# Kernel tuning notes

Measured on AMD Instinct MI355X. Metric: run time of the kernel, lower is better.

The kernel has to match this reference:

```python
import jax, jax.numpy as jnp
import numpy as np

B = 32          # graphs per batch
NPG = 512       # nodes per graph
EPG = 2048      # original edges per graph (stored in y[:, -1])
N = B * NPG     # 16384 nodes
E = B * EPG     # 65536 edges
GF = 5          # num_global_features
ETOT = E + N    # edges after add_self_loops

def _lin(k, o, i):
    return jax.random.normal(k, (o, i), jnp.float32) / np.sqrt(i)

def setup_inputs():
    key = jax.random.key(0)
    ks = jax.random.split(key, 20)
    x = jax.random.normal(ks[0], (N,), jnp.float32)
    off = (jnp.arange(B, dtype=jnp.int32) * NPG)[:, None]
    src = (jax.random.randint(ks[1], (B, EPG), 0, NPG, dtype=jnp.int32) + off).reshape(-1)
    dst = (jax.random.randint(ks[2], (B, EPG), 0, NPG, dtype=jnp.int32) + off).reshape(-1)
    edge_index = jnp.stack([src, dst])
    edge_attr = jax.random.normal(ks[3], (E, GF), jnp.float32)
    # last global feature = number of edges per graph (module reads y[:, -1])
    y = jax.random.normal(ks[4], (B, GF), jnp.float32).at[:, -1].set(float(EPG)).reshape(-1)
    batch_vector = jnp.repeat(jnp.arange(B, dtype=jnp.int32), NPG)
    p = dict(
        Wn=_lin(ks[5], 512, 1), bn=jnp.zeros(512, jnp.float32),
        We=_lin(ks[6], 511, GF), be=jnp.zeros(511, jnp.float32),
        Wg=_lin(ks[7], 512, GF), bg=jnp.zeros(512, jnp.float32),
        Wl=_lin(ks[8], 1024, 512), bl=jnp.zeros(1024, jnp.float32),
        Wr=_lin(ks[9], 1024, 512), br=jnp.zeros(1024, jnp.float32),
        Wge=_lin(ks[10], 1024, 511),
        att=jax.random.normal(ks[11], (1024,), jnp.float32) / 32.0,
        bgat=jnp.zeros(1024, jnp.float32),
        Wm=_lin(ks[12], 1024, 1024), bm=jnp.zeros(1024, jnp.float32),
        Wmi=_lin(ks[13], 1024, 1024), bmi=jnp.zeros(1024, jnp.float32),
        Wce=_lin(ks[14], 1024, 512), bce=jnp.zeros(1024, jnp.float32),
        W1=_lin(ks[15], 256, 2048), b1=jnp.zeros(256, jnp.float32),
        W2=_lin(ks[16], 1, 256), b2=jnp.zeros(1, jnp.float32),
    )
    return dict(x=x, edge_index=edge_index, edge_attr=edge_attr, y=y,
                batch_vector=batch_vector, **p)

def _leaky(v, s=0.01):
    return jnp.where(v >= 0, v, s * v)

def _forward(edge_index, batch_vector, x, edge_attr, y, Wn, bn, We, be, Wg, bg,
             Wl, bl, Wr, br, Wge, att, bgat, Wm, bm, Wmi, bmi, Wce, bce,
             W1, b1, W2, b2):
    # add_self_loops (fill_value=1.0 for edge_attr), self loops appended last
    loops = jnp.arange(N, dtype=edge_index.dtype)
    src = jnp.concatenate([edge_index[0], loops])
    dst = jnp.concatenate([edge_index[1], loops])
    ea = jnp.concatenate([edge_attr, jnp.ones((N, GF), edge_attr.dtype)], axis=0)
    # preprocessing MLPs (dropout = identity at inference)
    h = _leaky(x[:, None] @ Wn.T + bn)               # [N, 512]
    e = _leaky(ea @ We.T + be)                       # [ETOT, 511]
    yg = _leaky(y.reshape(B, GF) @ Wg.T + bg)        # [B, 512]
    # GATv2Conv, 1 head, concat, negative_slope=0.2, no self-loop add
    xl = h @ Wl.T + bl                               # source transform [N, 1024]
    xr = h @ Wr.T + br                               # target transform [N, 1024]
    m = _leaky(xl[src] + xr[dst] + e @ Wge.T, 0.2)   # [ETOT, 1024]
    logit = m @ att                                  # [ETOT]
    mx = jax.ops.segment_max(logit, dst, num_segments=N)
    ex = jnp.exp(logit - mx[dst])
    alpha = ex / (jax.ops.segment_sum(ex, dst, num_segments=N)[dst] + 1e-16)
    gat = jax.ops.segment_sum(alpha[:, None] * xl[src], dst, num_segments=N) + bgat
    edge_total = jnp.concatenate([e, alpha[:, None]], axis=1)  # [ETOT, 512]
    # GeneralConv: undirected message, add aggregation, identity skip (in==out)
    hm = gat @ Wm.T + bm
    hmi = gat @ Wmi.T + bmi
    eh = edge_total @ Wce.T + bce                    # [ETOT, 1024]
    deg = jax.ops.segment_sum(jnp.ones((ETOT,), gat.dtype), dst, num_segments=N)
    conv = (jax.ops.segment_sum(hm[src] + eh, dst, num_segments=N)
            + deg[:, None] * hmi + gat)              # [N, 1024]
    # global mean pooling (nodes) and module's contiguous edge batch vector
    nc = jax.ops.segment_sum(jnp.ones((N,), conv.dtype), batch_vector, num_segments=B)
    pn = jax.ops.segment_sum(conv, batch_vector, num_segments=B) / nc[:, None]
    ebatch = jnp.repeat(jnp.arange(B, dtype=jnp.int32), EPG + NPG)
    pe = jax.ops.segment_sum(edge_total, ebatch, num_segments=B) / float(EPG + NPG)
    pooled = jnp.concatenate([pn, pe, yg], axis=1)   # [B, 2048]
    out = _leaky(pooled @ W1.T + b1) @ W2.T + b2
    return jax.nn.sigmoid(out)                       # [B, 1]

def reference(x, edge_index, edge_attr, y, batch_vector, Wn, bn, We, be, Wg, bg,
              Wl, bl, Wr, br, Wge, att, bgat, Wm, bm, Wmi, bmi, Wce, bce,
              W1, b1, W2, b2):
    return _forward(edge_index, batch_vector, x, edge_attr, y, Wn, bn, We, be,
                    Wg, bg, Wl, bl, Wr, br, Wge, att, bgat, Wm, bm, Wmi, bmi,
                    Wce, bce, W1, b1, W2, b2)
```

## Files before the change

### kernel.cpp

```cpp
#include <hip/hip_runtime.h>
#include <cstdint>
#include <cstddef>

#define N_NODES 16384
#define N_EDGES 65536
#define ETOT    81920
#define B_GR    32

typedef __attribute__((ext_vector_type(8))) short bf16x8;
typedef __attribute__((ext_vector_type(4))) float f32x4;

static constexpr size_t OFF_XL    = 0;
static constexpr size_t OFF_XR    = 33554432ULL;
static constexpr size_t OFF_EBF   = 67108864ULL;
static constexpr size_t OFF_HBF   = 67108864ULL;
static constexpr size_t OFF_WCAT  = 83886080ULL;
static constexpr size_t OFF_WGEP  = 134217728ULL;
static constexpr size_t OFF_LOGIT = 135266304ULL;
static constexpr size_t OFF_DEG   = 135593984ULL;
static constexpr size_t OFF_ODEG  = 135659520ULL;
static constexpr size_t OFF_CURS  = 135725056ULL;
static constexpr size_t OFF_PG    = 135790592ULL;
static constexpr size_t OFF_PDG   = 135921664ULL;
static constexpr size_t OFF_PGAT  = 136052736ULL;
static constexpr size_t OFF_PS    = 136183808ULL;
static constexpr size_t OFF_PE    = 136249344ULL;
static constexpr size_t OFF_ROWP  = 136314880ULL;
static constexpr size_t OFF_CSR   = 136380672ULL;
static constexpr size_t OFF_ALPHA = 136708352ULL;
static constexpr size_t OFF_WLOOP = 137036032ULL;
static constexpr size_t OFF_YG    = 137040128ULL;
static constexpr size_t OFF_PN    = 137105664ULL;

__device__ __forceinline__ float leaky01(float v){ return v >= 0.f ? v : 0.01f*v; }
__device__ __forceinline__ float leaky02(float v){ return v >= 0.f ? v : 0.2f*v; }
__device__ __forceinline__ unsigned short f2bf(float f){
  union { float f; unsigned u; } v; v.f = f;
  unsigned r = v.u + 0x7FFFu + ((v.u >> 16) & 1u);
  return (unsigned short)(r >> 16);
}
__device__ __forceinline__ float bf2f(unsigned short h){
  union { unsigned u; float f; } v; v.u = ((unsigned)h) << 16;
  return v.f;
}

__global__ __launch_bounds__(256) void k_prep0(
    const float* __restrict__ x, const float* __restrict__ Wn, const float* __restrict__ bn,
    const float* __restrict__ Wl, const float* __restrict__ Wr,
    const float* __restrict__ Wge, const float* __restrict__ y,
    const float* __restrict__ Wg, const float* __restrict__ bg,
    const float* __restrict__ We, const float* __restrict__ be,
    float* __restrict__ zone, unsigned short* __restrict__ h_bf,
    unsigned short* __restrict__ Wcat, unsigned short* __restrict__ Wge_p,
    float* __restrict__ yg, float* __restrict__ we_loop) {
  __shared__ float e_lds[512];
  int bx = blockIdx.x, tid = threadIdx.x;
  if (bx < 256) {
    ((float4*)zone)[bx*256 + tid] = (float4){0.f,0.f,0.f,0.f};
  } else if (bx < 1280) {
    int gid = (bx-256)*256 + tid;
    int base = gid*8;
    int n = base >> 9, j = base & 511;
    float xv = x[n];
    float4 w0 = *(const float4*)(Wn + j);
    float4 w1 = *(const float4*)(Wn + j + 4);
    float4 b0 = *(const float4*)(bn + j);
    float4 b1 = *(const float4*)(bn + j + 4);
    unsigned short o[8];
    o[0]=f2bf(leaky01(xv*w0.x+b0.x)); o[1]=f2bf(leaky01(xv*w0.y+b0.y));
    o[2]=f2bf(leaky01(xv*w0.z+b0.z)); o[3]=f2bf(leaky01(xv*w0.w+b0.w));
    o[4]=f2bf(leaky01(xv*w1.x+b1.x)); o[5]=f2bf(leaky01(xv*w1.y+b1.y));
    o[6]=f2bf(leaky01(xv*w1.z+b1.z)); o[7]=f2bf(leaky01(xv*w1.w+b1.w));
    ((uint4*)h_bf)[gid] = *(const uint4*)o;
  } else if (bx < 2304) {
    int i = (bx-1280)*256 + tid;
    int base = i*4;
    const float* src = (base < 524288) ? (Wl + base) : (Wr + base - 524288);
    float4 v = *(const float4*)src;
    ushort4 o; o.x=f2bf(v.x); o.y=f2bf(v.y); o.z=f2bf(v.z); o.w=f2bf(v.w);
    ((ushort4*)Wcat)[i] = o;
  } else if (bx < 4352) {
    int gid = (bx-2304)*256 + tid;
    int j = gid >> 9, k = gid & 511;
    Wge_p[gid] = (k < 511) ? f2bf(Wge[(size_t)j*511 + k]) : (unsigned short)0;
  } else if (bx < 4416) {
    int gid = (bx-4352)*256 + tid;
    int b = gid >> 9, j = gid & 511;
    float s = bg[j];
    #pragma unroll
    for (int k=0;k<5;k++) s += y[b*5+k]*Wg[j*5+k];
    yg[gid] = leaky01(s);
  } else {
    for (int c = tid; c < 512; c += 256) {
      float v = 0.f;
      if (c < 511) {
        float s = be[c];
        #pragma unroll
        for (int q=0;q<5;q++) s += We[c*5+q];
        v = leaky01(s);
      }
      e_lds[c] = v;
    }
    __syncthreads();
    int j = (bx-4416)*256 + tid;
    float s = 0.f;
    for (int k=0;k<511;k++) s += e_lds[k]*Wge[(size_t)j*511+k];
    we_loop[j] = s;
  }
}

__global__ __launch_bounds__(256) void k_prep_e(
    const float* __restrict__ ea, const float* __restrict__ We, const float* __restrict__ be,
    unsigned short* __restrict__ E_bf) {
  int gid = blockIdx.x*256 + threadIdx.x;
  int e = gid >> 6, cg = gid & 63;
  int c0 = cg*8;
  const float* e5 = ea + (size_t)e*5;
  float a0=e5[0], a1=e5[1], a2=e5[2], a3=e5[3], a4=e5[4];
  unsigned short o[8];
  #pragma unroll
  for (int j=0;j<8;j++) {
    int c = c0 + j;
    float v = 0.f;
    if (c < 511) {
      const float* w = We + c*5;
      float s = be[c] + a0*w[0] + a1*w[1] + a2*w[2] + a3*w[3] + a4*w[4];
      v = leaky01(s);
    }
    o[j] = f2bf(v);
  }
  ((uint4*)E_bf)[gid] = *(const uint4*)o;
}

__global__ void k_deg(const int* __restrict__ ei, int* __restrict__ deg, int* __restrict__ odeg) {
  int i = blockIdx.x*blockDim.x + threadIdx.x;
  int s, d;
  if (i < N_EDGES) { s = ei[i]; d = ei[N_EDGES + i]; }
  else { s = i - N_EDGES; d = s; }
  atomicAdd(&deg[d], 1);
  atomicAdd(&odeg[s], 1);
}

__global__ __launch_bounds__(1024) void k_scan(const int* __restrict__ deg, int* __restrict__ rowptr) {
  __shared__ int sums[1024];
  int t = threadIdx.x;
  int local[16]; int s = 0;
  #pragma unroll
  for (int i=0;i<16;i++){ local[i] = deg[t*16+i]; s += local[i]; }
  sums[t] = s; __syncthreads();
  for (int off=1; off<1024; off<<=1) {
    int v = (t >= off) ? sums[t-off] : 0;
    __syncthreads();
    sums[t] += v;
    __syncthreads();
  }
  int run = (t==0) ? 0 : sums[t-1];
  if (t==0) rowptr[0] = 0;
  #pragma unroll
  for (int i=0;i<16;i++){ run += local[i]; rowptr[t*16+i+1] = run; }
}

__global__ void k_fill_csr(const int* __restrict__ ei, const int* __restrict__ rowptr,
                           int* __restrict__ cursor, int* __restrict__ csr) {
  int i = blockIdx.x*blockDim.x + threadIdx.x;
  int d = (i < N_EDGES) ? ei[N_EDGES + i] : (i - N_EDGES);
  int pos = rowptr[d] + atomicAdd(&cursor[d], 1);
  csr[pos] = i;
}

__global__ __launch_bounds__(256) void k_gemm_xlxr(
    const unsigned short* __restrict__ h_bf, const unsigned short* __restrict__ Wcat,
    const float* __restrict__ bl, const float* __restrict__ br,
    unsigned short* __restrict__ xl_bf, unsigned short* __restrict__ xr_bf) {
  __shared__ unsigned short As[128*40];
  __shared__ unsigned short Bs[128*40];
  int tid = threadIdx.x;
  int row0 = blockIdx.x*128, col0 = blockIdx.y*128;
  int w = tid >> 6, lane = tid & 63;
  int wm = w >> 1, wn = w & 1;
  int quad = lane >> 4, l16 = lane & 15;
  int sr = tid >> 1, skh = (tid & 1)*16;
  const unsigned short* ap = h_bf + (size_t)(row0+sr)*512 + skh;
  const unsigned short* wp = Wcat + (size_t)(col0+sr)*512 + skh;
  f32x4 acc[4][4];
  #pragma unroll
  for (int i=0;i<4;i++)
    #pragma unroll
    for (int j=0;j<4;j++) acc[i][j] = (f32x4){0.f,0.f,0.f,0.f};

  for (int k0 = 0; k0 < 512; k0 += 32) {
    uint4 a0 = *(const uint4*)(ap + k0);
    uint4 a1 = *(const uint4*)(ap + k0 + 8);
    uint4 b0 = *(const uint4*)(wp + k0);
    uint4 b1 = *(const uint4*)(wp + k0 + 8);
    *(uint4*)&As[sr*40 + skh]     = a0;
    *(uint4*)&As[sr*40 + skh + 8] = a1;
    *(uint4*)&Bs[sr*40 + skh]     = b0;
    *(uint4*)&Bs[sr*40 + skh + 8] = b1;
    __syncthreads();
    bf16x8 af[4], bfr[4];
    #pragma unroll
    for (int mi=0;mi<4;mi++)
      af[mi] = *(const bf16x8*)&As[(wm*64 + mi*16 + l16)*40 + quad*8];
    #pragma unroll
    for (int ni=0;ni<4;ni++)
      bfr[ni] = *(const bf16x8*)&Bs[(wn*64 + ni*16 + l16)*40 + quad*8];
    #pragma unroll
    for (int mi=0;mi<4;mi++)
      #pragma unroll
      for (int ni=0;ni<4;ni++)
        acc[mi][ni] = __builtin_amdgcn_mfma_f32_16x16x32_bf16(af[mi], bfr[ni], acc[mi][ni], 0, 0, 0);
    __syncthreads();
  }
  bool isL = (blockIdx.y < 8);
  const float* bias = isL ? bl : br;
  unsigned short* O = isL ? xl_bf : xr_bf;
  int cb = isL ? col0 : (col0 - 1024);
  float bias4[4];
  #pragma unroll
  for (int ni=0;ni<4;ni++) bias4[ni] = bias[cb + wn*64 + ni*16 + l16];
  #pragma unroll
  for (int mi=0;mi<4;mi++)
    #pragma unroll
    for (int ni=0;ni<4;ni++) {
      int col = cb + wn*64 + ni*16 + l16;
      #pragma unroll
      for (int r=0;r<4;r++) {
        int row = row0 + wm*64 + mi*16 + quad*4 + r;
        O[(size_t)row*1024 + col] = f2bf(acc[mi][ni][r] + bias4[ni]);
      }
    }
}

__global__ __launch_bounds__(256) void k_mfma_we(
    const unsigned short* __restrict__ E_bf, const unsigned short* __restrict__ Wge_bf,
    const int* __restrict__ ei,
    const unsigned short* __restrict__ xl_bf, const unsigned short* __restrict__ xr_bf,
    const float* __restrict__ att, float* __restrict__ logit) {
  __shared__ unsigned short As[128*40];
  __shared__ unsigned short Bs[128*40];
  int tid = threadIdx.x;
  int row0 = blockIdx.x*128, col0 = blockIdx.y*128;
  int w = tid >> 6, lane = tid & 63;
  int wm = w >> 1, wn = w & 1;
  int quad = lane >> 4, l16 = lane & 15;
  int sr = tid >> 1, skh = (tid & 1)*16;
  const unsigned short* ap = E_bf  + (size_t)(row0+sr)*512 + skh;
  const unsigned short* wp = Wge_bf + (size_t)(col0+sr)*512 + skh;
  f32x4 acc[4][4];
  #pragma unroll
  for (int i=0;i<4;i++)
    #pragma unroll
    for (int j=0;j<4;j++) acc[i][j] = (f32x4){0.f,0.f,0.f,0.f};

  for (int k0 = 0; k0 < 512; k0 += 32) {
    uint4 a0 = *(const uint4*)(ap + k0);
    uint4 a1 = *(const uint4*)(ap + k0 + 8);
    uint4 b0 = *(const uint4*)(wp + k0);
    uint4 b1 = *(const uint4*)(wp + k0 + 8);
    *(uint4*)&As[sr*40 + skh]     = a0;
    *(uint4*)&As[sr*40 + skh + 8] = a1;
    *(uint4*)&Bs[sr*40 + skh]     = b0;
    *(uint4*)&Bs[sr*40 + skh + 8] = b1;
    __syncthreads();
    bf16x8 af[4], bfr[4];
    #pragma unroll
    for (int mi=0;mi<4;mi++)
      af[mi] = *(const bf16x8*)&As[(wm*64 + mi*16 + l16)*40 + quad*8];
    #pragma unroll
    for (int ni=0;ni<4;ni++)
      bfr[ni] = *(const bf16x8*)&Bs[(wn*64 + ni*16 + l16)*40 + quad*8];
    #pragma unroll
    for (int mi=0;mi<4;mi++)
      #pragma unroll
      for (int ni=0;ni<4;ni++)
        acc[mi][ni] = __builtin_amdgcn_mfma_f32_16x16x32_bf16(af[mi], bfr[ni], acc[mi][ni], 0, 0, 0);
    __syncthreads();
  }
  float att4[4];
  #pragma unroll
  for (int ni=0;ni<4;ni++) att4[ni] = att[col0 + wn*64 + ni*16 + l16];
  #pragma unroll
  for (int mi=0;mi<4;mi++) {
    #pragma unroll
    for (int r=0;r<4;r++) {
      int e = row0 + wm*64 + mi*16 + quad*4 + r;
      int s = ei[e], d = ei[N_EDGES + e];
      const unsigned short* xlr = xl_bf + (size_t)s*1024;
      const unsigned short* xrr = xr_bf + (size_t)d*1024;
      float p = 0.f;
      #pragma unroll
      for (int ni=0;ni<4;ni++) {
        int col = col0 + wn*64 + ni*16 + l16;
        float z = acc[mi][ni][r] + bf2f(xlr[col]) + bf2f(xrr[col]);
        z = leaky02(z);
        p += z*att4[ni];
      }
      p += __shfl_down(p, 8, 16);
      p += __shfl_down(p, 4, 16);
      p += __shfl_down(p, 2, 16);
      p += __shfl_down(p, 1, 16);
      if (l16 == 0) atomicAdd(&logit[e], p);
    }
  }
}

__global__ __launch_bounds__(256) void k_softmax_gat(
    const int* __restrict__ ei, const int* __restrict__ rowptr, const int* __restrict__ csr,
    const float* __restrict__ logit,
    const unsigned short* __restrict__ xl_bf, const unsigned short* __restrict__ xr_bf,
    const float* __restrict__ we_loop, const float* __restrict__ att,
    const float* __restrict__ bgat,
    float* __restrict__ alpha, unsigned short* __restrict__ gat_bf) {
  __shared__ float sl[256];
  __shared__ int   se[256];
  __shared__ float red[256];
  int n = blockIdx.x, tid = threadIdx.x;
  {
    ushort4 a = ((const ushort4*)(xl_bf + (size_t)n*1024))[tid];
    ushort4 b = ((const ushort4*)(xr_bf + (size_t)n*1024))[tid];
    float4 c = ((const float4*)we_loop)[tid];
    float4 t = ((const float4*)att)[tid];
    float s = 0.f;
    s += leaky02(bf2f(a.x)+bf2f(b.x)+c.x)*t.x;
    s += leaky02(bf2f(a.y)+bf2f(b.y)+c.y)*t.y;
    s += leaky02(bf2f(a.z)+bf2f(b.z)+c.z)*t.z;
    s += leaky02(bf2f(a.w)+bf2f(b.w)+c.w)*t.w;
    red[tid] = s;
  }
  __syncthreads();
  #pragma unroll
  for (int off=128; off; off>>=1){ if (tid<off) red[tid] += red[tid+off]; __syncthreads(); }
  float sll = red[0];
  __syncthreads();

  int beg = rowptr[n], end = rowptr[n+1], cnt = end - beg;
  float m = -1e30f;
  for (int p = beg+tid; p < end; p += 256) {
    int e = csr[p];
    float lg = (e < N_EDGES) ? logit[e] : sll;
    int idx = p - beg;
    if (idx < 256) { se[idx] = e; sl[idx] = lg; }
    m = fmaxf(m, lg);
  }
  red[tid] = m; __syncthreads();
  #pragma unroll
  for (int off=128; off; off>>=1){ if (tid<off) red[tid] = fmaxf(red[tid], red[tid+off]); __syncthreads(); }
  m = red[0];
  __syncthreads();
  float ss = 0.f;
  for (int p = beg+tid; p < end; p += 256) {
    int idx = p - beg;
    float lg;
    if (idx < 256) lg = sl[idx];
    else { int e = csr[p]; lg = (e < N_EDGES) ? logit[e] : sll; }
    ss += expf(lg - m);
  }
  red[tid] = ss; __syncthreads();
  #pragma unroll
  for (int off=128; off; off>>=1){ if (tid<off) red[tid] += red[tid+off]; __syncthreads(); }
  float inv = 1.f/(red[0] + 1e-16f);
  __syncthreads();
  for (int p = beg+tid; p < end; p += 256) {
    int idx = p - beg;
    int e; float lg;
    if (idx < 256) { e = se[idx]; lg = sl[idx]; }
    else { e = csr[p]; lg = (e < N_EDGES) ? logit[e] : sll; }
    float a = expf(lg - m)*inv;
    alpha[e] = a;
    if (idx < 256) sl[idx] = a;
  }
  __syncthreads();
  float4 acc = ((const float4*)bgat)[tid];
  for (int p = 0; p < cnt; p++) {
    float a; int e;
    if (p < 256) { a = sl[p]; e = se[p]; }
    else { e = csr[beg+p]; float lg = (e < N_EDGES) ? logit[e] : sll; a = expf(lg - m)*inv; }
    int s = (e < N_EDGES) ? ei[e] : (e - N_EDGES);
    ushort4 v = ((const ushort4*)(xl_bf + (size_t)s*1024))[tid];
    acc.x += a*bf2f(v.x); acc.y += a*bf2f(v.y); acc.z += a*bf2f(v.z); acc.w += a*bf2f(v.w);
  }
  ushort4 o; o.x=f2bf(acc.x); o.y=f2bf(acc.y); o.z=f2bf(acc.z); o.w=f2bf(acc.w);
  ((ushort4*)(gat_bf + (size_t)n*1024))[tid] = o;
}

__global__ __launch_bounds__(256) void k_nodepool(
    const unsigned short* __restrict__ gat_bf, const int* __restrict__ odeg,
    const int* __restrict__ rowptr,
    float* __restrict__ P_G, float* __restrict__ P_DG, float* __restrict__ P_gat) {
  int b = blockIdx.x, yy = blockIdx.y;
  int nc = yy >> 2, cg = yy & 3;
  int col = cg*256 + threadIdx.x;
  float a1=0.f, a2=0.f, a3=0.f;
  int n0 = b*512 + nc*128;
  for (int i=0;i<128;i++){
    int n = n0 + i;
    float g = bf2f(gat_bf[(size_t)n*1024 + col]);
    float od = (float)odeg[n];
    float dg = (float)(rowptr[n+1]-rowptr[n]);
    a1 += od*g; a2 += dg*g; a3 += g;
  }
  atomicAdd(&P_G[b*1024+col], a1);
  atomicAdd(&P_DG[b*1024+col], a2);
  atomicAdd(&P_gat[b*1024+col], a3);
}

__global__ __launch_bounds__(256) void k_edgepool(
    const float* __restrict__ ea, const float* __restrict__ We, const float* __restrict__ be,
    const float* __restrict__ alpha, float* __restrict__ P_S, float* __restrict__ pe, int mode) {
  __shared__ float sea[640];
  __shared__ float sal[128];
  int b = blockIdx.x, ch = blockIdx.y, tid = threadIdx.x;
  int c1 = tid, c2 = tid + 256;
  bool v2 = (c2 < 511);
  float w1[5], w2[5]={0,0,0,0,0}, b1v, b2v=0.f;
  #pragma unroll
  for (int q=0;q<5;q++) w1[q] = We[c1*5+q];
  b1v = be[c1];
  if (v2) {
    #pragma unroll
    for (int q=0;q<5;q++) w2[q] = We[c2*5+q];
    b2v = be[c2];
  }
  int base = (mode == 0)
    ? ((ch < 16) ? (b*2048 + ch*128) : (N_EDGES + b*512 + (ch-16)*128))
    : (b*2560 + ch*128);
  for (int i=tid;i<640;i+=256){
    int r = base + i/5;
    sea[i] = (r < N_EDGES) ? ea[(size_t)r*5 + (i%5)] : 1.0f;
  }
  for (int i=tid;i<128;i+=256) sal[i] = alpha[base + i];
  __syncthreads();
  float acc1 = 0.f, acc2 = 0.f;
  for (int rr=0; rr<128; rr++) {
    const float* er = &sea[rr*5];
    acc1 += leaky01(b1v + er[0]*w1[0]+er[1]*w1[1]+er[2]*w1[2]+er[3]*w1[3]+er[4]*w1[4]);
    if (v2) acc2 += leaky01(b2v + er[0]*w2[0]+er[1]*w2[1]+er[2]*w2[2]+er[3]*w2[3]+er[4]*w2[4]);
    else    acc2 += sal[rr];
  }
  if (mode == 0) {
    atomicAdd(&P_S[b*512+c1], acc1);
    atomicAdd(&P_S[b*512+c2], acc2);
  } else {
    const float sc = 1.f/2560.f;
    atomicAdd(&pe[b*512+c1], acc1*sc);
    atomicAdd(&pe[b*512+c2], acc2*sc);
  }
}

__global__ __launch_bounds__(256) void k_pn(
    const float* __restrict__ P_G, const float* __restrict__ P_DG,
    const float* __restrict__ P_S, const float* __restrict__ P_gat,
    const float* __restrict__ Wm, const float* __restrict__ bm,
    const float* __restrict__ Wmi, const float* __restrict__ bmi,
    const float* __restrict__ Wce, const float* __restrict__ bce,
    float* __restrict__ pn) {
  __shared__ float sPg[1024], sPdg[1024], sPs[512];
  int b = blockIdx.x, col0 = blockIdx.y*64;
  int tid = threadIdx.x, w = tid >> 6, lane = tid & 63;
  for (int i=tid;i<1024;i+=256){ sPg[i]=P_G[b*1024+i]; sPdg[i]=P_DG[b*1024+i]; }
  for (int i=tid;i<512;i+=256) sPs[i]=P_S[b*512+i];
  __syncthreads();
  for (int c=0;c<16;c++){
    int j = col0 + w*16 + c;
    const float* wm  = Wm  + (size_t)j*1024;
    const float* wmi = Wmi + (size_t)j*1024;
    const float* wce = Wce + (size_t)j*512;
    float s = 0.f;
    #pragma unroll 4
    for (int i=0;i<16;i++){ int k = lane + i*64; s += sPg[k]*wm[k] + sPdg[k]*wmi[k]; }
    #pragma unroll 4
    for (int i=0;i<8;i++){ int k = lane + i*64; s += sPs[k]*wce[k]; }
    #pragma unroll
    for (int off=32; off; off>>=1) s += __shfl_down(s, off);
    if (lane == 0) {
      pn[b*1024+j] = (s + P_gat[b*1024+j] + 2560.f*(bm[j]+bmi[j]+bce[j])) * (1.f/512.f);
    }
  }
}

__global__ __launch_bounds__(256) void k_final(
    const float* __restrict__ pn, const float* __restrict__ pe, const float* __restrict__ yg,
    const float* __restrict__ W1, const float* __restrict__ b1,
    const float* __restrict__ W2, const float* __restrict__ b2,
    float* __restrict__ out) {
  __shared__ float pooled[2048];
  __shared__ float red[256];
  int b = blockIdx.x, tid = threadIdx.x;
  for (int i=tid;i<1024;i+=256) pooled[i]      = pn[b*1024+i];
  for (int i=tid;i<512;i+=256)  pooled[1024+i] = pe[b*512+i];
  for (int i=tid;i<512;i+=256)  pooled[1536+i] = yg[b*512+i];
  __syncthreads();
  const float4* w4 = (const float4*)(W1 + (size_t)tid*2048);
  const float4* p4 = (const float4*)pooled;
  float s = b1[tid];
  for (int k=0;k<512;k++){
    float4 w = w4[k]; float4 p = p4[k];
    s += w.x*p.x + w.y*p.y + w.z*p.z + w.w*p.w;
  }
  s = leaky01(s);
  red[tid] = s * W2[tid];
  __syncthreads();
  for (int off=128; off; off>>=1){
    if (tid < off) red[tid] += red[tid+off];
    __syncthreads();
  }
  if (tid == 0){
    float o = red[0] + b2[0];
    out[b] = 1.f/(1.f+expf(-o));
  }
}

extern "C" void kernel_launch(void* const* d_in, const int* in_sizes, int n_in,
                              void* d_out, int out_size, void* d_ws, size_t ws_size,
                              hipStream_t stream) {
  const float* x   = (const float*)d_in[0];
  const int*   ei  = (const int*)  d_in[1];
  const float* ea  = (const float*)d_in[2];
  const float* y   = (const float*)d_in[3];
  const float* Wn  = (const float*)d_in[5];
  const float* bn  = (const float*)d_in[6];
  const float* We  = (const float*)d_in[7];
  const float* be  = (const float*)d_in[8];
  const float* Wg  = (const float*)d_in[9];
  const float* bg  = (const float*)d_in[10];
  const float* Wl  = (const float*)d_in[11];
  const float* bl  = (const float*)d_in[12];
  const float* Wr  = (const float*)d_in[13];
  const float* br  = (const float*)d_in[14];
  const float* Wge = (const float*)d_in[15];
  const float* att = (const float*)d_in[16];
  const float* bgat= (const float*)d_in[17];
  const float* Wm  = (const float*)d_in[18];
  const float* bm  = (const float*)d_in[19];
  const float* Wmi = (const float*)d_in[20];
  const float* bmi = (const float*)d_in[21];
  const float* Wce = (const float*)d_in[22];
  const float* bce = (const float*)d_in[23];
  const float* W1  = (const float*)d_in[24];
  const float* b1  = (const float*)d_in[25];
  const float* W2  = (const float*)d_in[26];
  const float* b2  = (const float*)d_in[27];
  float* out = (float*)d_out;

  char* ws = (char*)d_ws;
  unsigned short* xl_bf  = (unsigned short*)(ws + OFF_XL);
  unsigned short* xr_bf  = (unsigned short*)(ws + OFF_XR);
  unsigned short* gat_bf = (unsigned short*)(ws + OFF_XR);
  unsigned short* E_bf   = (unsigned short*)(ws + OFF_EBF);
  unsigned short* h_bf   = (unsigned short*)(ws + OFF_HBF);
  unsigned short* Wcat   = (unsigned short*)(ws + OFF_WCAT);
  unsigned short* Wge_p  = (unsigned short*)(ws + OFF_WGEP);
  float* zone   = (float*)(ws + OFF_LOGIT);
  float* logit  = (float*)(ws + OFF_LOGIT);
  int*   deg    = (int*)  (ws + OFF_DEG);
  int*   odeg   = (int*)  (ws + OFF_ODEG);
  int*   cursor = (int*)  (ws + OFF_CURS);
  float* P_G    = (float*)(ws + OFF_PG);
  float* P_DG   = (float*)(ws + OFF_PDG);
  float* P_gat  = (float*)(ws + OFF_PGAT);
  float* P_S    = (float*)(ws + OFF_PS);
  float* pe     = (float*)(ws + OFF_PE);
  int*   rowptr = (int*)  (ws + OFF_ROWP);
  int*   csr    = (int*)  (ws + OFF_CSR);
  float* alpha  = (float*)(ws + OFF_ALPHA);
  float* we_loop= (float*)(ws + OFF_WLOOP);
  float* yg     = (float*)(ws + OFF_YG);
  float* pn     = (float*)(ws + OFF_PN);

  k_prep0<<<dim3(4420), dim3(256), 0, stream>>>(x, Wn, bn, Wl, Wr, Wge, y, Wg, bg, We, be,
                                                zone, h_bf, Wcat, Wge_p, yg, we_loop);
  k_deg<<<dim3(320), dim3(256), 0, stream>>>(ei, deg, odeg);
  k_scan<<<dim3(1), dim3(1024), 0, stream>>>(deg, rowptr);
  k_fill_csr<<<dim3(320), dim3(256), 0, stream>>>(ei, rowptr, cursor, csr);
  k_gemm_xlxr<<<dim3(128,16), dim3(256), 0, stream>>>(h_bf, Wcat, bl, br, xl_bf, xr_bf);
  k_prep_e<<<dim3(16384), dim3(256), 0, stream>>>(ea, We, be, E_bf);
  k_mfma_we<<<dim3(512,8), dim3(256), 0, stream>>>(E_bf, Wge_p, ei, xl_bf, xr_bf, att, logit);
  k_softmax_gat<<<dim3(16384), dim3(256), 0, stream>>>(ei, rowptr, csr, logit, xl_bf, xr_bf,
                                                       we_loop, att, bgat, alpha, gat_bf);
  k_nodepool<<<dim3(32,16), dim3(256), 0, stream>>>(gat_bf, odeg, rowptr, P_G, P_DG, P_gat);
  k_edgepool<<<dim3(32,20), dim3(256), 0, stream>>>(ea, We, be, alpha, P_S, pe, 0);
  k_edgepool<<<dim3(32,20), dim3(256), 0, stream>>>(ea, We, be, alpha, P_S, pe, 1);
  k_pn<<<dim3(32,16), dim3(256), 0, stream>>>(P_G, P_DG, P_S, P_gat, Wm, bm, Wmi, bmi, Wce, bce, pn);
  k_final<<<dim3(32), dim3(256), 0, stream>>>(pn, pe, yg, W1, b1, W2, b2, out);
}
```

Measured before the change: 660.5 us.

## Load GEMM tiles directly into LDS via global_load_lds in both MFMA kernels

Replaces the register-staged global-to-LDS copies in the two bf16 MFMA GEMMs with direct global_load_lds transfers. The LDS layout is changed to the MFMA fragment order, so each wave's 16-row by 32-k slab sits contiguously and the padded 40-stride layout is no longer needed. The 2D grid is also flattened to 1D, with column tiles varying fastest, which changes the order in which blocks touch memory. This is meant to cut VGPR use and remove the load-then-store instruction pair per tile. The loop still has no double buffering, so load latency remains exposed behind the barrier.

Result: slower. 687.0 us (+4.0%).

```diff
diff --git a/kernel.cpp b/kernel.cpp
--- a/kernel.cpp
+++ b/kernel.cpp
@@ -9,6 +9,9 @@
 
 typedef __attribute__((ext_vector_type(8))) short bf16x8;
 typedef __attribute__((ext_vector_type(4))) float f32x4;
+
+#define AS1 __attribute__((address_space(1)))
+#define AS3 __attribute__((address_space(3)))
 
 static constexpr size_t OFF_XL    = 0;
 static constexpr size_t OFF_XR    = 33554432ULL;
@@ -168,20 +171,27 @@
   csr[pos] = i;
 }
 
+
 __global__ __launch_bounds__(256) void k_gemm_xlxr(
     const unsigned short* __restrict__ h_bf, const unsigned short* __restrict__ Wcat,
     const float* __restrict__ bl, const float* __restrict__ br,
     unsigned short* __restrict__ xl_bf, unsigned short* __restrict__ xr_bf) {
-  __shared__ unsigned short As[128*40];
-  __shared__ unsigned short Bs[128*40];
+  __shared__ unsigned short As[4096];
+  __shared__ unsigned short Bs[4096];
+  int blk = blockIdx.x;
+  int bx = blk >> 4, by = blk & 15;
+  int row0 = bx*128, col0 = by*128;
   int tid = threadIdx.x;
-  int row0 = blockIdx.x*128, col0 = blockIdx.y*128;
   int w = tid >> 6, lane = tid & 63;
   int wm = w >> 1, wn = w & 1;
   int quad = lane >> 4, l16 = lane & 15;
-  int sr = tid >> 1, skh = (tid & 1)*16;
-  const unsigned short* ap = h_bf + (size_t)(row0+sr)*512 + skh;
-  const unsigned short* wp = Wcat + (size_t)(col0+sr)*512 + skh;
+  int ks = lane >> 4;
+  size_t a0off = (size_t)(row0 + w*16 + l16)*512 + ks*8;
+  size_t b0off = (size_t)(col0 + w*16 + l16)*512 + ks*8;
+  unsigned short* lA0 = As + (size_t)w*512;
+  unsigned short* lA1 = As + 2048 + (size_t)w*512;
+  unsigned short* lB0 = Bs + (size_t)w*512;
+  unsigned short* lB1 = Bs + 2048 + (size_t)w*512;
   f32x4 acc[4][4];
   #pragma unroll
   for (int i=0;i<4;i++)
@@ -189,22 +199,18 @@
     for (int j=0;j<4;j++) acc[i][j] = (f32x4){0.f,0.f,0.f,0.f};
 
   for (int k0 = 0; k0 < 512; k0 += 32) {
-    uint4 a0 = *(const uint4*)(ap + k0);
-    uint4 a1 = *(const uint4*)(ap + k0 + 8);
-    uint4 b0 = *(const uint4*)(wp + k0);
-    uint4 b1 = *(const uint4*)(wp + k0 + 8);
-    *(uint4*)&As[sr*40 + skh]     = a0;
-    *(uint4*)&As[sr*40 + skh + 8] = a1;
-    *(uint4*)&Bs[sr*40 + skh]     = b0;
-    *(uint4*)&Bs[sr*40 + skh + 8] = b1;
+    __builtin_amdgcn_global_load_lds((const AS1 void*)(h_bf + a0off + k0),           (AS3 void*)lA0, 16, 0, 0);
+    __builtin_amdgcn_global_load_lds((const AS1 void*)(h_bf + a0off + 64*512 + k0),  (AS3 void*)lA1, 16, 0, 0);
+    __builtin_amdgcn_global_load_lds((const AS1 void*)(Wcat + b0off + k0),           (AS3 void*)lB0, 16, 0, 0);
+    __builtin_amdgcn_global_load_lds((const AS1 void*)(Wcat + b0off + 64*512 + k0),  (AS3 void*)lB1, 16, 0, 0);
     __syncthreads();
     bf16x8 af[4], bfr[4];
     #pragma unroll
     for (int mi=0;mi<4;mi++)
-      af[mi] = *(const bf16x8*)&As[(wm*64 + mi*16 + l16)*40 + quad*8];
+      af[mi] = *(const bf16x8*)&As[(size_t)(((wm*4+mi)*64 + quad*16 + l16))*8];
     #pragma unroll
     for (int ni=0;ni<4;ni++)
-      bfr[ni] = *(const bf16x8*)&Bs[(wn*64 + ni*16 + l16)*40 + quad*8];
+      bfr[ni] = *(const bf16x8*)&Bs[(size_t)(((wn*4+ni)*64 + quad*16 + l16))*8];
     #pragma unroll
     for (int mi=0;mi<4;mi++)
       #pragma unroll
@@ -212,7 +218,7 @@
         acc[mi][ni] = __builtin_amdgcn_mfma_f32_16x16x32_bf16(af[mi], bfr[ni], acc[mi][ni], 0, 0, 0);
     __syncthreads();
   }
-  bool isL = (blockIdx.y < 8);
+  bool isL = (by < 8);
   const float* bias = isL ? bl : br;
   unsigned short* O = isL ? xl_bf : xr_bf;
   int cb = isL ? col0 : (col0 - 1024);
@@ -237,16 +243,22 @@
     const int* __restrict__ ei,
     const unsigned short* __restrict__ xl_bf, const unsigned short* __restrict__ xr_bf,
     const float* __restrict__ att, float* __restrict__ logit) {
-  __shared__ unsigned short As[128*40];
-  __shared__ unsigned short Bs[128*40];
+  __shared__ unsigned short As[4096];
+  __shared__ unsigned short Bs[4096];
+  int blk = blockIdx.x;
+  int bx = blk >> 3, by = blk & 7;
+  int row0 = bx*128, col0 = by*128;
   int tid = threadIdx.x;
-  int row0 = blockIdx.x*128, col0 = blockIdx.y*128;
   int w = tid >> 6, lane = tid & 63;
   int wm = w >> 1, wn = w & 1;
   int quad = lane >> 4, l16 = lane & 15;
-  int sr = tid >> 1, skh = (tid & 1)*16;
-  const unsigned short* ap = E_bf  + (size_t)(row0+sr)*512 + skh;
-  const unsigned short* wp = Wge_bf + (size_t)(col0+sr)*512 + skh;
+  int ks = lane >> 4;
+  size_t a0off = (size_t)(row0 + w*16 + l16)*512 + ks*8;
+  size_t b0off = (size_t)(col0 + w*16 + l16)*512 + ks*8;
+  unsigned short* lA0 = As + (size_t)w*512;
+  unsigned short* lA1 = As + 2048 + (size_t)w*512;
+  unsigned short* lB0 = Bs + (size_t)w*512;
+  unsigned short* lB1 = Bs + 2048 + (size_t)w*512;
   f32x4 acc[4][4];
   #pragma unroll
   for (int i=0;i<4;i++)
@@ -254,22 +266,18 @@
     for (int j=0;j<4;j++) acc[i][j] = (f32x4){0.f,0.f,0.f,0.f};
 
   for (int k0 = 0; k0 < 512; k0 += 32) {
-    uint4 a0 = *(const uint4*)(ap + k0);
-    uint4 a1 = *(const uint4*)(ap + k0 + 8);
-    uint4 b0 = *(const uint4*)(wp + k0);
-    uint4 b1 = *(const uint4*)(wp + k0 + 8);
-    *(uint4*)&As[sr*40 + skh]     = a0;
-    *(uint4*)&As[sr*40 + skh + 8] = a1;
-    *(uint4*)&Bs[sr*40 + skh]     = b0;
-    *(uint4*)&Bs[sr*40 + skh + 8] = b1;
+    __builtin_amdgcn_global_load_lds((const AS1 void*)(E_bf + a0off + k0),            (AS3 void*)lA0, 16, 0, 0);
+    __builtin_amdgcn_global_load_lds((const AS1 void*)(E_bf + a0off + 64*512 + k0),   (AS3 void*)lA1, 16, 0, 0);
+    __builtin_amdgcn_global_load_lds((const AS1 void*)(Wge_bf + b0off + k0),          (AS3 void*)lB0, 16, 0, 0);
+    __builtin_amdgcn_global_load_lds((const AS1 void*)(Wge_bf + b0off + 64*512 + k0), (AS3 void*)lB1, 16, 0, 0);
     __syncthreads();
     bf16x8 af[4], bfr[4];
     #pragma unroll
     for (int mi=0;mi<4;mi++)
-      af[mi] = *(const bf16x8*)&As[(wm*64 + mi*16 + l16)*40 + quad*8];
+      af[mi] = *(const bf16x8*)&As[(size_t)(((wm*4+mi)*64 + quad*16 + l16))*8];
     #pragma unroll
     for (int ni=0;ni<4;ni++)
-      bfr[ni] = *(const bf16x8*)&Bs[(wn*64 + ni*16 + l16)*40 + quad*8];
+      bfr[ni] = *(const bf16x8*)&Bs[(size_t)(((wn*4+ni)*64 + quad*16 + l16))*8];
     #pragma unroll
     for (int mi=0;mi<4;mi++)
       #pragma unroll
@@ -573,9 +581,9 @@
   k_deg<<<dim3(320), dim3(256), 0, stream>>>(ei, deg, odeg);
   k_scan<<<dim3(1), dim3(1024), 0, stream>>>(deg, rowptr);
   k_fill_csr<<<dim3(320), dim3(256), 0, stream>>>(ei, rowptr, cursor, csr);
-  k_gemm_xlxr<<<dim3(128,16), dim3(256), 0, stream>>>(h_bf, Wcat, bl, br, xl_bf, xr_bf);
+  k_gemm_xlxr<<<dim3(2048), dim3(256), 0, stream>>>(h_bf, Wcat, bl, br, xl_bf, xr_bf);
   k_prep_e<<<dim3(16384), dim3(256), 0, stream>>>(ea, We, be, E_bf);
-  k_mfma_we<<<dim3(512,8), dim3(256), 0, stream>>>(E_bf, Wge_p, ei, xl_bf, xr_bf, att, logit);
+  k_mfma_we<<<dim3(4096), dim3(256), 0, stream>>>(E_bf, Wge_p, ei, xl_bf, xr_bf, att, logit);
   k_softmax_gat<<<dim3(16384), dim3(256), 0, stream>>>(ei, rowptr, csr, logit, xl_bf, xr_bf,
                                                        we_loop, att, bgat, alpha, gat_bf);
   k_nodepool<<<dim3(32,16), dim3(256), 0, stream>>>(gat_bf, odeg, rowptr, P_G, P_DG, P_gat);
```
